# Optimization experiments

Measured on AMD Instinct MI355X. Metric: run time of the kernel, lower is better.

The kernel has to match this reference:

```python
import jax, jax.numpy as jnp
import numpy as np

N_NODES = 20000
N_ATTRS = 5000
IN_FEATURES = 512
OUT_FEATURES = 128
ALPHA = 0.2  # LeakyReLU negative slope
NEG_INF = -9e15


def setup_inputs() -> dict:
    key = jax.random.key(0)
    k1, k2, k3, k4, k5 = jax.random.split(key, 5)
    node_embedding = jax.random.normal(k1, (N_NODES, IN_FEATURES), dtype=jnp.float32)
    attr_embedding = jax.random.normal(k2, (N_ATTRS, IN_FEATURES), dtype=jnp.float32)
    feat_mat = jax.random.randint(k3, (N_NODES, N_ATTRS), 0, 2, dtype=jnp.int32)
    # xavier_uniform with gain=1.414 (as in torch init)
    gain = 1.414
    lim_W = gain * np.sqrt(6.0 / (IN_FEATURES + OUT_FEATURES))
    W = jax.random.uniform(k4, (IN_FEATURES, OUT_FEATURES), minval=-lim_W, maxval=lim_W, dtype=jnp.float32)
    lim_a = gain * np.sqrt(6.0 / (2 * OUT_FEATURES + 1))
    a = jax.random.uniform(k5, (2 * OUT_FEATURES, 1), minval=-lim_a, maxval=lim_a, dtype=jnp.float32)
    return {"node_embedding": node_embedding, "attr_embedding": attr_embedding,
            "feat_mat": feat_mat, "W": W, "a": a}


def reference(node_embedding, attr_embedding, feat_mat, W, a):
    # Linear projections
    node_h = node_embedding @ W            # [N, F]
    attr_h = attr_embedding @ W            # [M, F]
    # Additive attention scores: e[i,j] = leakyrelu(a1.node_h[i] + a2.attr_h[j])
    wh1 = node_h @ a[:OUT_FEATURES, :]     # [N, 1]
    wh2 = attr_h @ a[OUT_FEATURES:, :]     # [M, 1]
    e = jax.nn.leaky_relu(wh1 + wh2.T, negative_slope=ALPHA)  # [N, M]
    # Mask where there is no node-attribute link, then softmax over attrs
    attention = jnp.where(feat_mat > 0, e, NEG_INF)
    attention = jax.nn.softmax(attention, axis=1)
    # (dropout is identity in eval mode)
    h_prime = attention @ attr_h           # [N, F]
    return jax.nn.elu(h_prime)             # concat=True branch
```

## Files before the change

### kernel.cpp

```cpp
#include <hip/hip_runtime.h>

#define N_NODES 20000
#define N_ATTRS 5000
#define IN_F    512
#define OUT_F   128
#define KP      5120
#define KSTEPS  160
#define NSS     80
#define WH2_PAD 5376
#define NEGBIG  -1e30f
#define LOG2E   1.4426950408889634f

typedef _Float16 f16x8 __attribute__((ext_vector_type(8)));
typedef float    f32x4 __attribute__((ext_vector_type(4)));
typedef int      i32x4 __attribute__((ext_vector_type(4)));

__device__ __forceinline__ float fast_exp2(float x) {
    return __builtin_amdgcn_exp2f(x);
}

__device__ __forceinline__ void async16(void* lds_dst, const void* gsrc) {
    __builtin_amdgcn_global_load_lds(
        (const __attribute__((address_space(1))) unsigned int*)gsrc,
        (__attribute__((address_space(3))) unsigned int*)lds_dst, 16, 0, 0);
}

__device__ __forceinline__ unsigned fkey(float f) {
    unsigned b = __float_as_uint(f);
    return (b & 0x80000000u) ? ~b : (b | 0x80000000u);
}
__device__ __forceinline__ float funkey(unsigned u) {
    unsigned b = (u & 0x80000000u) ? (u ^ 0x80000000u) : ~u;
    return __uint_as_float(b);
}

__global__ __launch_bounds__(256) void prep_kernel(
    const float* __restrict__ W, const float* __restrict__ a,
    float* __restrict__ Wa1, float* __restrict__ Wa2, _Float16* __restrict__ Wp,
    unsigned* __restrict__ maxu) {
    int gt = blockIdx.x * blockDim.x + threadIdx.x;
    if (gt == 0) maxu[0] = 0u;
    if (gt < IN_F) {
        int k = gt;
        float s1 = 0.f, s2 = 0.f;
        for (int f = 0; f < OUT_F; ++f) {
            float w = W[k * OUT_F + f];
            s1 += w * a[f];
            s2 += w * a[OUT_F + f];
        }
        Wa1[k] = s1 * LOG2E;
        Wa2[k] = s2 * LOG2E;
    }
    for (int idx = gt; idx < IN_F * OUT_F; idx += gridDim.x * blockDim.x) {
        int j    = idx & 7;
        int lane = (idx >> 3) & 63;
        int nb   = (idx >> 9) & 7;
        int kb   = idx >> 12;
        int k = kb * 32 + (lane >> 4) * 8 + j;
        int n = nb * 16 + (lane & 15);
        Wp[idx] = (_Float16)W[k * OUT_F + n];
    }
}

__global__ __launch_bounds__(256) void wh_kernel(
    const float* __restrict__ node_emb, const float* __restrict__ attr_emb,
    const float* __restrict__ Wa1, const float* __restrict__ Wa2,
    float* __restrict__ wh1, float* __restrict__ wh2,
    unsigned* __restrict__ maxu) {
    __shared__ float red[4];
    int wave = threadIdx.x >> 6, lane = threadIdx.x & 63;
    int r = blockIdx.x * 4 + wave;
    const float* src;
    const float* vec;
    float* dst;
    if (r < N_NODES) {
        src = node_emb + (size_t)r * IN_F; vec = Wa1; dst = wh1 + r;
    } else {
        int r2 = r - N_NODES;
        src = attr_emb + (size_t)r2 * IN_F; vec = Wa2; dst = wh2 + r2;
    }
    float4 ra = *reinterpret_cast<const float4*>(src + lane * 8);
    float4 rb = *reinterpret_cast<const float4*>(src + lane * 8 + 4);
    const float* vp = vec + lane * 8;
    float s = ra.x * vp[0] + ra.y * vp[1] + ra.z * vp[2] + ra.w * vp[3]
            + rb.x * vp[4] + rb.y * vp[5] + rb.z * vp[6] + rb.w * vp[7];
#pragma unroll
    for (int off = 1; off < 64; off <<= 1) s += __shfl_xor(s, off, 64);
    if (lane == 0) *dst = s;

    if (blockIdx.x == 0) {
        for (int j = N_ATTRS + threadIdx.x; j < WH2_PAD; j += 256) wh2[j] = NEGBIG;
    }
    if (blockIdx.x >= 5000) {
        if (lane == 0) red[wave] = s;
        __syncthreads();
        if (threadIdx.x == 0) {
            float m4 = fmaxf(fmaxf(red[0], red[1]), fmaxf(red[2], red[3]));
            atomicMax(maxu, fkey(m4));
        }
    }
}

__global__ __launch_bounds__(64) void attr_h_kernel(
    const float* __restrict__ attr_emb, const _Float16* __restrict__ Wp,
    _Float16* __restrict__ Vp) {
    int lane = threadIdx.x & 63;
    int m = lane & 15, quad = lane >> 4;
    int j0 = blockIdx.x * 16;
    int j = j0 + m;
    bool valid = j < N_ATTRS;
    f32x4 acc[8];
#pragma unroll
    for (int nb = 0; nb < 8; ++nb)
#pragma unroll
        for (int t = 0; t < 4; ++t) acc[nb][t] = 0.f;
    const float* arow = attr_emb + (size_t)j * IN_F;
    for (int kk = 0; kk < IN_F / 32; ++kk) {
        f16x8 afrag;
        if (valid) {
            float4 ra = *reinterpret_cast<const float4*>(arow + kk * 32 + quad * 8);
            float4 rb = *reinterpret_cast<const float4*>(arow + kk * 32 + quad * 8 + 4);
            afrag[0] = (_Float16)ra.x; afrag[1] = (_Float16)ra.y;
            afrag[2] = (_Float16)ra.z; afrag[3] = (_Float16)ra.w;
            afrag[4] = (_Float16)rb.x; afrag[5] = (_Float16)rb.y;
            afrag[6] = (_Float16)rb.z; afrag[7] = (_Float16)rb.w;
        } else {
#pragma unroll
            for (int t = 0; t < 8; ++t) afrag[t] = (_Float16)0.f;
        }
        const _Float16* wbase = Wp + (size_t)(kk * 8) * 64 * 8;
#pragma unroll
        for (int nb = 0; nb < 8; ++nb) {
            f16x8 bfrag;
            __builtin_memcpy(&bfrag, wbase + (nb * 64 + lane) * 8, 16);
            acc[nb] = __builtin_amdgcn_mfma_f32_16x16x32_f16(afrag, bfrag, acc[nb], 0, 0, 0);
        }
    }
#pragma unroll
    for (int nb = 0; nb < 8; ++nb) {
#pragma unroll
        for (int reg = 0; reg < 4; ++reg) {
            int jr = j0 + quad * 4 + reg;
            float v = (jr < N_ATTRS) ? acc[nb][reg] : 0.f;
            size_t idx = ((size_t)((jr >> 5) * 8 + nb) * 64 +
                          (((jr >> 3) & 3) * 16 + m)) * 8 + (jr & 7);
            Vp[idx] = (_Float16)v;
        }
    }
}

__global__ __launch_bounds__(256, 3) void attn_kernel(
    const int* __restrict__ feat, const float* __restrict__ wh1,
    const float* __restrict__ wh2, const unsigned* __restrict__ maxu,
    const _Float16* __restrict__ Vp, float* __restrict__ out) {
    __shared__ __align__(16) char lds[49664];
    __shared__ float rsums[32];

    int wave = threadIdx.x >> 6, lane = threadIdx.x & 63;
    int m = lane & 15, quad = lane >> 4;
    int i0 = blockIdx.x * 32;
    int rg = (wave >> 1) * 16;
    int half = wave & 1;

    float wh1i = wh1[i0 + rg + m];
    float emax = wh1i + funkey(maxu[0]);
    float Mi = fmaxf(emax, 0.2f * emax) - 12.f;

    f32x4 acc[8];
#pragma unroll
    for (int nb = 0; nb < 8; ++nb)
#pragma unroll
        for (int t = 0; t < 4; ++t) acc[nb][t] = 0.f;
    float s = 0.f;

    char* vbuf0 = lds;
    char* fbuf0 = lds + 32768;
    char* wbuf0 = lds + 49152;

    const char* featb = (const char*)feat;
    size_t frow_off = (size_t)(i0 + rg + m) * N_ATTRS * 4;

    auto stage = [&](int ss, int b) {
        const char* vsrc = (const char*)Vp + (size_t)ss * 16384 + wave * 4096 + lane * 16;
        char* vdst = vbuf0 + b * 16384 + wave * 4096;
#pragma unroll
        for (int q = 0; q < 4; ++q) async16(vdst + q * 1024, vsrc + q * 1024);
        int kbase = (2 * ss + half) * 32;
        char* fdst = fbuf0 + b * 8192 + wave * 2048;
#pragma unroll
        for (int h = 0; h < 2; ++h) {
            int a = kbase + quad * 8 + h * 4;
            a = min(a, N_ATTRS - 4);
            async16(fdst + h * 1024, featb + frow_off + (size_t)a * 4);
        }
        if (wave == 0 && lane < 16)
            async16(wbuf0 + b * 256, (const char*)(wh2 + ss * 64) + lane * 16);
    };

    stage(0, 0);
    __syncthreads();

    for (int ss = 0; ss < NSS; ++ss) {
        int cur = ss & 1;
        if (ss + 1 < NSS) stage(ss + 1, cur ^ 1);

        char* wb = wbuf0 + cur * 256 + half * 128 + quad * 32;
        float4 wva = *reinterpret_cast<const float4*>(wb);
        float4 wvb = *reinterpret_cast<const float4*>(wb + 16);
        char* fb = fbuf0 + cur * 8192 + wave * 2048 + lane * 16;
        i32x4 fA = *reinterpret_cast<const i32x4*>(fb);
        i32x4 fB = *reinterpret_cast<const i32x4*>(fb + 1024);

        int   fi[8] = {fA.x, fA.y, fA.z, fA.w, fB.x, fB.y, fB.z, fB.w};
        float wv[8] = {wva.x, wva.y, wva.z, wva.w, wvb.x, wvb.y, wvb.z, wvb.w};
        f16x8 afrag;
#pragma unroll
        for (int t = 0; t < 8; ++t) {
            float e = wh1i + wv[t];
            float l = fmaxf(e, 0.2f * e);
            float p = fast_exp2(l - Mi);
            p = (fi[t] > 0) ? p : 0.f;
            _Float16 ph = (_Float16)p;
            s += (float)ph;
            afrag[t] = ph;
        }

        char* vb = vbuf0 + cur * 16384 + half * 8192;
#pragma unroll
        for (int nb = 0; nb < 8; ++nb) {
            f16x8 bfrag = *reinterpret_cast<const f16x8*>(vb + nb * 1024 + lane * 16);
            acc[nb] = __builtin_amdgcn_mfma_f32_16x16x32_f16(afrag, bfrag, acc[nb], 0, 0, 0);
        }

        __syncthreads();
    }

    s += __shfl_xor(s, 16, 64);
    s += __shfl_xor(s, 32, 64);

    float* accp = (float*)lds;
    if (half == 0) {
#pragma unroll
        for (int nb = 0; nb < 8; ++nb)
#pragma unroll
            for (int reg = 0; reg < 4; ++reg)
                accp[(rg + quad * 4 + reg) * 128 + nb * 16 + m] = acc[nb][reg];
        if (lane < 16) rsums[rg + lane] = s;
    }
    __syncthreads();
    if (half == 1) {
#pragma unroll
        for (int nb = 0; nb < 8; ++nb)
#pragma unroll
            for (int reg = 0; reg < 4; ++reg)
                accp[(rg + quad * 4 + reg) * 128 + nb * 16 + m] += acc[nb][reg];
        if (lane < 16) rsums[rg + lane] += s;
    }
    __syncthreads();

    for (int o = threadIdx.x; o < 32 * 128; o += 256) {
        int lr = o >> 7, n = o & 127;
        float v = accp[lr * 128 + n];
        float rs = rsums[lr];
        rs = (rs > 0.f) ? rs : 1.f;
        float h = v / rs;
        float ov = (h > 0.f) ? h : (fast_exp2(h * LOG2E) - 1.f);
        out[(size_t)(i0 + lr) * OUT_F + n] = ov;
    }
}

extern "C" void kernel_launch(void* const* d_in, const int* in_sizes, int n_in,
                              void* d_out, int out_size, void* d_ws, size_t ws_size,
                              hipStream_t stream) {
    const float* node_emb = (const float*)d_in[0];
    const float* attr_emb = (const float*)d_in[1];
    const int*   feat     = (const int*)d_in[2];
    const float* W        = (const float*)d_in[3];
    const float* a        = (const float*)d_in[4];
    float*       out      = (float*)d_out;

    char* ws = (char*)d_ws;
    float*    Wa1 = (float*)(ws + 0);
    float*    Wa2 = (float*)(ws + 4096);
    float*    wh1 = (float*)(ws + 8192);
    float*    wh2 = (float*)(ws + 90112);
    unsigned* mxu = (unsigned*)(ws + 111616);
    _Float16* Wp  = (_Float16*)(ws + 131072);
    _Float16* Vp  = (_Float16*)(ws + 262144);

    prep_kernel<<<64, 256, 0, stream>>>(W, a, Wa1, Wa2, Wp, mxu);
    wh_kernel<<<6250, 256, 0, stream>>>(node_emb, attr_emb, Wa1, Wa2, wh1, wh2, mxu);
    attr_h_kernel<<<320, 64, 0, stream>>>(attr_emb, Wp, Vp);
    attn_kernel<<<625, 256, 0, stream>>>(feat, wh1, wh2, mxu, Vp, out);
}
```

Before: 656.9 us.

## Load V and wh2 fragments directly from global, stage only feat in LDS

The attention kernel stops staging the packed V matrix and wh2 through LDS. Each wave now reads its B-fragments and wh2 values straight from global memory (likely L2-resident), and only the feat mask goes through async LDS copies, in a 4-slot ring processed two sub-steps per barrier. LDS use drops from about 49KB to 32KB, launch bounds rise to 4 blocks per SM, and barriers are halved. The trade-off is exposed global-load latency on V with no explicit prefetch, plus more register pressure from holding 8 fragments.

Measured after the change: 688.8 us. 4.9% more time.

```diff
diff --git a/kernel.cpp b/kernel.cpp
--- a/kernel.cpp
+++ b/kernel.cpp
@@ -7,6 +7,7 @@
 #define KP      5120
 #define KSTEPS  160
 #define NSS     80
+#define NPAIR   40
 #define WH2_PAD 5376
 #define NEGBIG  -1e30f
 #define LOG2E   1.4426950408889634f
@@ -149,11 +150,11 @@
     }
 }
 
-__global__ __launch_bounds__(256, 3) void attn_kernel(
+__global__ __launch_bounds__(256, 4) void attn_kernel(
     const int* __restrict__ feat, const float* __restrict__ wh1,
     const float* __restrict__ wh2, const unsigned* __restrict__ maxu,
     const _Float16* __restrict__ Vp, float* __restrict__ out) {
-    __shared__ __align__(16) char lds[49664];
+    __shared__ __align__(16) char lds[32768];
     __shared__ float rsums[32];
 
     int wave = threadIdx.x >> 6, lane = threadIdx.x & 63;
@@ -173,41 +174,32 @@
         for (int t = 0; t < 4; ++t) acc[nb][t] = 0.f;
     float s = 0.f;
 
-    char* vbuf0 = lds;
-    char* fbuf0 = lds + 32768;
-    char* wbuf0 = lds + 49152;
-
     const char* featb = (const char*)feat;
     size_t frow_off = (size_t)(i0 + rg + m) * N_ATTRS * 4;
 
-    auto stage = [&](int ss, int b) {
-        const char* vsrc = (const char*)Vp + (size_t)ss * 16384 + wave * 4096 + lane * 16;
-        char* vdst = vbuf0 + b * 16384 + wave * 4096;
-#pragma unroll
-        for (int q = 0; q < 4; ++q) async16(vdst + q * 1024, vsrc + q * 1024);
+    auto stageF = [&](int ss) {
         int kbase = (2 * ss + half) * 32;
-        char* fdst = fbuf0 + b * 8192 + wave * 2048;
+        char* fdst = lds + (ss & 3) * 8192 + wave * 2048;
 #pragma unroll
         for (int h = 0; h < 2; ++h) {
             int a = kbase + quad * 8 + h * 4;
             a = min(a, N_ATTRS - 4);
             async16(fdst + h * 1024, featb + frow_off + (size_t)a * 4);
         }
-        if (wave == 0 && lane < 16)
-            async16(wbuf0 + b * 256, (const char*)(wh2 + ss * 64) + lane * 16);
     };
 
-    stage(0, 0);
-    __syncthreads();
-
-    for (int ss = 0; ss < NSS; ++ss) {
-        int cur = ss & 1;
-        if (ss + 1 < NSS) stage(ss + 1, cur ^ 1);
-
-        char* wb = wbuf0 + cur * 256 + half * 128 + quad * 32;
-        float4 wva = *reinterpret_cast<const float4*>(wb);
-        float4 wvb = *reinterpret_cast<const float4*>(wb + 16);
-        char* fb = fbuf0 + cur * 8192 + wave * 2048 + lane * 16;
+    auto computeSS = [&](int ss) {
+        int k = 2 * ss + half;
+        const _Float16* vb = Vp + (size_t)k * 4096 + lane * 8;
+        f16x8 bf[8];
+#pragma unroll
+        for (int nb = 0; nb < 8; ++nb)
+            bf[nb] = *reinterpret_cast<const f16x8*>(vb + nb * 512);
+        const float* wp = wh2 + k * 32 + quad * 8;
+        float4 wva = *reinterpret_cast<const float4*>(wp);
+        float4 wvb = *reinterpret_cast<const float4*>(wp + 4);
+
+        const char* fb = lds + (ss & 3) * 8192 + wave * 2048 + lane * 16;
         i32x4 fA = *reinterpret_cast<const i32x4*>(fb);
         i32x4 fB = *reinterpret_cast<const i32x4*>(fb + 1024);
 
@@ -224,14 +216,18 @@
             s += (float)ph;
             afrag[t] = ph;
         }
-
-        char* vb = vbuf0 + cur * 16384 + half * 8192;
-#pragma unroll
-        for (int nb = 0; nb < 8; ++nb) {
-            f16x8 bfrag = *reinterpret_cast<const f16x8*>(vb + nb * 1024 + lane * 16);
-            acc[nb] = __builtin_amdgcn_mfma_f32_16x16x32_f16(afrag, bfrag, acc[nb], 0, 0, 0);
-        }
-
+#pragma unroll
+        for (int nb = 0; nb < 8; ++nb)
+            acc[nb] = __builtin_amdgcn_mfma_f32_16x16x32_f16(afrag, bf[nb], acc[nb], 0, 0, 0);
+    };
+
+    stageF(0); stageF(1);
+    __syncthreads();
+
+    for (int p = 0; p < NPAIR; ++p) {
+        if (p + 1 < NPAIR) { stageF(2 * p + 2); stageF(2 * p + 3); }
+        computeSS(2 * p);
+        computeSS(2 * p + 1);
         __syncthreads();
     }
 
```
